# Performance work log

Measured on AMD Instinct MI355X. Metric: run time of the kernel, lower is better.

The kernel has to match this reference:

```python
import jax, jax.numpy as jnp
import numpy as np

N_NODES = 50000
N_EDGES = 800000
IN_CH = 128
OUT_CH = 32
HID = 2 * OUT_CH  # 64


def setup_inputs() -> dict:
    key = jax.random.key(0)
    ks = jax.random.split(key, 8)
    x = jax.random.normal(ks[0], (N_NODES, IN_CH), dtype=jnp.float32)
    edge_index = jax.random.randint(ks[1], (2, N_EDGES), 0, N_NODES, dtype=jnp.int32)
    s1 = 1.0 / np.sqrt(IN_CH)
    s2 = 1.0 / np.sqrt(HID)
    W1 = jax.random.normal(ks[2], (IN_CH, HID), dtype=jnp.float32) * s1
    b1 = jnp.zeros((HID,), dtype=jnp.float32)
    W_mu = jax.random.normal(ks[3], (HID, OUT_CH), dtype=jnp.float32) * s2
    b_mu = jnp.zeros((OUT_CH,), dtype=jnp.float32)
    W_logstd = jax.random.normal(ks[4], (HID, OUT_CH), dtype=jnp.float32) * s2
    b_logstd = jnp.zeros((OUT_CH,), dtype=jnp.float32)
    return {"x": x, "edge_index": edge_index, "W1": W1, "b1": b1,
            "W_mu": W_mu, "b_mu": b_mu, "W_logstd": W_logstd, "b_logstd": b_logstd}


def _gcn_norm(edge_index, n, dtype):
    # PyG GCNConv: add self-loops, symmetric normalization D^-1/2 A D^-1/2
    loops = jnp.arange(n, dtype=edge_index.dtype)
    src = jnp.concatenate([edge_index[0], loops])
    dst = jnp.concatenate([edge_index[1], loops])
    deg = jax.ops.segment_sum(jnp.ones_like(dst, dtype=dtype), dst, num_segments=n)
    deg_inv_sqrt = jnp.where(deg > 0, jax.lax.rsqrt(deg), 0.0)
    norm = deg_inv_sqrt[src] * deg_inv_sqrt[dst]  # [E+N]
    return src, dst, norm


def _gcn_conv(x, W, b, src, dst, norm, n):
    h = x @ W                        # transform first (in >= out)
    msg = h[src] * norm[:, None]     # gather + scale, [E+N, out]
    out = jax.ops.segment_sum(msg, dst, num_segments=n)
    return out + b


def reference(x, edge_index, W1, b1, W_mu, b_mu, W_logstd, b_logstd):
    n = x.shape[0]
    src, dst, norm = _gcn_norm(edge_index, n, x.dtype)
    h = jax.nn.relu(_gcn_conv(x, W1, b1, src, dst, norm, n))
    mu = _gcn_conv(h, W_mu, b_mu, src, dst, norm, n)
    logstd = _gcn_conv(h, W_logstd, b_logstd, src, dst, norm, n)
    return mu, logstd
```

## Files before the change

### kernel.cpp

```cpp
#include <hip/hip_runtime.h>
#include <hip/hip_fp16.h>

#define N_NODES 50000
#define N_EDGES 800000
#define IN_CH 128
#define HID 64
#define OUT_CH 32
#define CAP 64
#define ZROW N_NODES
#define PART_SZ 6250

union H4 { uint2 u; __half2 h[2]; };

__global__ __launch_bounds__(256) void k_scatter(const int* __restrict__ ei,
                                                 int* cur, unsigned short* __restrict__ pk,
                                                 unsigned* zA, unsigned* zB) {
    if (blockIdx.x == 0) {
        int t = threadIdx.x;
        if (t < 32) zA[t] = 0u;
        else if (t < 64) zB[t - 32] = 0u;
    }
    int part = blockIdx.x & 7;
    int g = (blockIdx.x >> 3) * 256 + threadIdx.x;
    if (g >= N_EDGES / 2) return;
    int2 dd = ((const int2*)(ei + N_EDGES))[g];
    bool a0 = (unsigned)(dd.x - part * PART_SZ) < (unsigned)PART_SZ;
    bool a1 = (unsigned)(dd.y - part * PART_SZ) < (unsigned)PART_SZ;
    if (!a0 && !a1) return;
    int2 ss = ((const int2*)ei)[g];
    if (a0) {
        int n = atomicAdd(&cur[dd.x], 1);
        int slot = (n < 32) ? (((n & 7) << 2) | (n >> 3)) : n;
        pk[(dd.x << 6) + slot] = (unsigned short)ss.x;
    }
    if (a1) {
        int n = atomicAdd(&cur[dd.y], 1);
        int slot = (n < 32) ? (((n & 7) << 2) | (n >> 3)) : n;
        pk[(dd.y << 6) + slot] = (unsigned short)ss.y;
    }
}

__global__ __launch_bounds__(256) void k_mm1(const float* __restrict__ x,
                                             const float* __restrict__ W1,
                                             const int* __restrict__ cur,
                                             __half* __restrict__ t1) {
    __shared__ float4 ws[64 * 16];
    __shared__ float  xsT[64 * 64];
    int t = threadIdx.x;
    int n0 = blockIdx.x * 64;
    int lane = t & 63, wv_ = t >> 6;
    int ni = lane >> 2;
    int cq = ((lane & 3) << 2) + wv_;
    const float4* W4 = (const float4*)W1;
    const float4* x4 = (const float4*)x;
    float4 acc0 = {0,0,0,0}, acc1 = acc0, acc2 = acc0, acc3 = acc0;
#pragma unroll
    for (int kt = 0; kt < 2; ++kt) {
        __syncthreads();
#pragma unroll
        for (int i = 0; i < 4; ++i) {
            int L = i * 256 + t;
            ws[L] = W4[kt * 1024 + L];
            int n = L >> 4, q = L & 15;
            int ng = n0 + n; if (ng >= N_NODES) ng = N_NODES - 1;
            float4 v = x4[ng * 32 + kt * 16 + q];
            int fb = q * 256 + (((n >> 2) ^ q) << 2) + (n & 3);
            xsT[fb]       = v.x;
            xsT[fb + 64]  = v.y;
            xsT[fb + 128] = v.z;
            xsT[fb + 192] = v.w;
        }
        __syncthreads();
        const float4* xsT4 = (const float4*)xsT;
#pragma unroll 8
        for (int k = 0; k < 64; ++k) {
            float4 xv = xsT4[k * 16 + (ni ^ (k >> 2))];
            float4 wvv = ws[k * 16 + cq];
            acc0.x += xv.x * wvv.x; acc0.y += xv.x * wvv.y; acc0.z += xv.x * wvv.z; acc0.w += xv.x * wvv.w;
            acc1.x += xv.y * wvv.x; acc1.y += xv.y * wvv.y; acc1.z += xv.y * wvv.z; acc1.w += xv.y * wvv.w;
            acc2.x += xv.z * wvv.x; acc2.y += xv.z * wvv.y; acc2.z += xv.z * wvv.z; acc2.w += xv.z * wvv.w;
            acc3.x += xv.w * wvv.x; acc3.y += xv.w * wvv.y; acc3.z += xv.w * wvv.z; acc3.w += xv.w * wvv.w;
        }
    }
    int nb = n0 + 4 * ni;
    if (nb < N_NODES) {
        int4 c4 = *(const int4*)(cur + nb);
        float d0 = rsqrtf((float)c4.x + 1.0f);
        float d1 = rsqrtf((float)c4.y + 1.0f);
        float d2 = rsqrtf((float)c4.z + 1.0f);
        float d3 = rsqrtf((float)c4.w + 1.0f);
        uint2* o2 = (uint2*)t1;
        H4 v;
        v.h[0] = __floats2half2_rn(d0 * acc0.x, d0 * acc0.y);
        v.h[1] = __floats2half2_rn(d0 * acc0.z, d0 * acc0.w);
        o2[(nb + 0) * 16 + cq] = v.u;
        v.h[0] = __floats2half2_rn(d1 * acc1.x, d1 * acc1.y);
        v.h[1] = __floats2half2_rn(d1 * acc1.z, d1 * acc1.w);
        o2[(nb + 1) * 16 + cq] = v.u;
        v.h[0] = __floats2half2_rn(d2 * acc2.x, d2 * acc2.y);
        v.h[1] = __floats2half2_rn(d2 * acc2.z, d2 * acc2.w);
        o2[(nb + 2) * 16 + cq] = v.u;
        v.h[0] = __floats2half2_rn(d3 * acc3.x, d3 * acc3.y);
        v.h[1] = __floats2half2_rn(d3 * acc3.z, d3 * acc3.w);
        o2[(nb + 3) * 16 + cq] = v.u;
    }
}

__global__ __launch_bounds__(256) void k_agg(const unsigned short* __restrict__ pk,
                                             const int* __restrict__ cur,
                                             const __half* __restrict__ in,
                                             const float* __restrict__ bias,
                                             __half* __restrict__ out,
                                             int apply_relu) {
    int w = (blockIdx.x * 256 + threadIdx.x) >> 6;
    if (w >= N_NODES) return;
    int lane = threadIdx.x & 63;
    int eg = lane >> 3, cs = lane & 7;
    int cnt = __builtin_amdgcn_readfirstlane(cur[w]);
    int rowb = w << 6;
    const uint4* __restrict__ inv = (const uint4*)in;
    float acc[8] = {0,0,0,0,0,0,0,0};

    uint2 pp = *(const uint2*)(pk + rowb + (eg << 2));
    int s0 = (eg      < cnt) ? (int)(pp.x & 0xffff) : ZROW;
    int s1 = (8 + eg  < cnt) ? (int)(pp.x >> 16)    : ZROW;
    int s2 = (16 + eg < cnt) ? (int)(pp.y & 0xffff) : ZROW;
    int s3 = (24 + eg < cnt) ? (int)(pp.y >> 16)    : ZROW;
    uint4 r0 = inv[s0 * 8 + cs];
    uint4 r1 = inv[s1 * 8 + cs];
    uint4 r2 = inv[s2 * 8 + cs];
    uint4 r3 = inv[s3 * 8 + cs];
#define ACC8(R) { const __half2* h2 = (const __half2*)&(R); float2 f;          \
        f = __half22float2(h2[0]); acc[0] += f.x; acc[1] += f.y;               \
        f = __half22float2(h2[1]); acc[2] += f.x; acc[3] += f.y;               \
        f = __half22float2(h2[2]); acc[4] += f.x; acc[5] += f.y;               \
        f = __half22float2(h2[3]); acc[6] += f.x; acc[7] += f.y; }
    ACC8(r0); ACC8(r1); ACC8(r2); ACC8(r3);

    for (int base = 32; base < cnt; base += 8) {
        int je = base + eg;
        int s = (je < cnt) ? (int)pk[rowb + je] : ZROW;
        uint4 r = inv[s * 8 + cs];
        ACC8(r);
    }
#undef ACC8
#pragma unroll
    for (int m = 8; m <= 32; m <<= 1)
#pragma unroll
        for (int i = 0; i < 8; ++i) acc[i] += __shfl_xor(acc[i], m, 64);
    if (eg == 0) {
        uint4 sr = inv[w * 8 + cs];
        const __half2* sh = (const __half2*)&sr;
        float2 f;
        f = __half22float2(sh[0]); acc[0] += f.x; acc[1] += f.y;
        f = __half22float2(sh[1]); acc[2] += f.x; acc[3] += f.y;
        f = __half22float2(sh[2]); acc[4] += f.x; acc[5] += f.y;
        f = __half22float2(sh[3]); acc[6] += f.x; acc[7] += f.y;
        float dw = rsqrtf((float)cnt + 1.0f);
        if (apply_relu) {
            float4 b0 = ((const float4*)bias)[2 * cs];
            float4 b1v = ((const float4*)bias)[2 * cs + 1];
            acc[0] = dw * fmaxf(dw * acc[0] + b0.x, 0.f);
            acc[1] = dw * fmaxf(dw * acc[1] + b0.y, 0.f);
            acc[2] = dw * fmaxf(dw * acc[2] + b0.z, 0.f);
            acc[3] = dw * fmaxf(dw * acc[3] + b0.w, 0.f);
            acc[4] = dw * fmaxf(dw * acc[4] + b1v.x, 0.f);
            acc[5] = dw * fmaxf(dw * acc[5] + b1v.y, 0.f);
            acc[6] = dw * fmaxf(dw * acc[6] + b1v.z, 0.f);
            acc[7] = dw * fmaxf(dw * acc[7] + b1v.w, 0.f);
        } else {
#pragma unroll
            for (int i = 0; i < 8; ++i) acc[i] *= dw;
        }
        __half2 o[4];
        o[0] = __floats2half2_rn(acc[0], acc[1]);
        o[1] = __floats2half2_rn(acc[2], acc[3]);
        o[2] = __floats2half2_rn(acc[4], acc[5]);
        o[3] = __floats2half2_rn(acc[6], acc[7]);
        ((uint4*)out)[w * 8 + cs] = *(const uint4*)o;
    }
}

__global__ __launch_bounds__(256) void k_mm2(const __half* __restrict__ agg2,
                                             const float* __restrict__ Wmu,
                                             const float* __restrict__ bmu,
                                             const float* __restrict__ Wls,
                                             const float* __restrict__ bls,
                                             float* __restrict__ out) {
    __shared__ float4 ws[64 * 16];
    __shared__ float  xsT[64 * 64];
    int t = threadIdx.x;
    int n0 = blockIdx.x * 64;
    int lane = t & 63, wv_ = t >> 6;
    int ni = lane >> 2;
    int cq = ((lane & 3) << 2) + wv_;
    const float4* Wm4 = (const float4*)Wmu;
    const float4* Wl4 = (const float4*)Wls;
    const uint2*  x2  = (const uint2*)agg2;
#pragma unroll
    for (int i = 0; i < 4; ++i) {
        int L = i * 256 + t;
        int k = L >> 4, c = L & 15;
        ws[L] = (c < 8) ? Wm4[k * 8 + c] : Wl4[k * 8 + (c - 8)];
        int n = L >> 4, q = L & 15;
        int ng = n0 + n; if (ng >= N_NODES) ng = N_NODES - 1;
        H4 hv; hv.u = x2[ng * 16 + q];
        float2 f0 = __half22float2(hv.h[0]), f1 = __half22float2(hv.h[1]);
        int fb = q * 256 + (((n >> 2) ^ q) << 2) + (n & 3);
        xsT[fb]       = f0.x;
        xsT[fb + 64]  = f0.y;
        xsT[fb + 128] = f1.x;
        xsT[fb + 192] = f1.y;
    }
    float4 b = (cq < 8) ? ((const float4*)bmu)[cq] : ((const float4*)bls)[cq - 8];
    float4 acc0 = b, acc1 = b, acc2 = b, acc3 = b;
    __syncthreads();
    const float4* xsT4 = (const float4*)xsT;
#pragma unroll 8
    for (int k = 0; k < 64; ++k) {
        float4 xv = xsT4[k * 16 + (ni ^ (k >> 2))];
        float4 wvv = ws[k * 16 + cq];
        acc0.x += xv.x * wvv.x; acc0.y += xv.x * wvv.y; acc0.z += xv.x * wvv.z; acc0.w += xv.x * wvv.w;
        acc1.x += xv.y * wvv.x; acc1.y += xv.y * wvv.y; acc1.z += xv.y * wvv.z; acc1.w += xv.y * wvv.w;
        acc2.x += xv.z * wvv.x; acc2.y += xv.z * wvv.y; acc2.z += xv.z * wvv.z; acc2.w += xv.z * wvv.w;
        acc3.x += xv.w * wvv.x; acc3.y += xv.w * wvv.y; acc3.z += xv.w * wvv.z; acc3.w += xv.w * wvv.w;
    }
    int nb = n0 + 4 * ni;
    if (nb < N_NODES) {
        float4* o4 = (float4*)out;
        long base_off = (cq < 8) ? 0 : (long)N_NODES * 8;
        int cq8 = cq & 7;
        o4[base_off + (long)(nb + 0) * 8 + cq8] = acc0;
        o4[base_off + (long)(nb + 1) * 8 + cq8] = acc1;
        o4[base_off + (long)(nb + 2) * 8 + cq8] = acc2;
        o4[base_off + (long)(nb + 3) * 8 + cq8] = acc3;
    }
}

extern "C" void kernel_launch(void* const* d_in, const int* in_sizes, int n_in,
                              void* d_out, int out_size, void* d_ws, size_t ws_size,
                              hipStream_t stream) {
    const float* x   = (const float*)d_in[0];
    const int*   ei  = (const int*)  d_in[1];
    const float* W1  = (const float*)d_in[2];
    const float* b1  = (const float*)d_in[3];
    const float* Wmu = (const float*)d_in[4];
    const float* bmu = (const float*)d_in[5];
    const float* Wls = (const float*)d_in[6];
    const float* bls = (const float*)d_in[7];
    float* out = (float*)d_out;

    int*   cur  = (int*)d_ws;
    unsigned short* pk = (unsigned short*)((int*)d_ws + 50176);
    __half* bufA = (__half*)((int*)d_ws + 1650176);
    __half* bufB = (__half*)((int*)d_ws + 3250304);
    __half* bufC = (__half*)((int*)d_ws + 4850432);

    hipMemsetAsync(d_ws, 0, 200000, stream);
    k_scatter <<<1563 * 8, 256, 0, stream>>>(ei, cur, pk,
                   (unsigned*)(bufA + (size_t)ZROW * HID),
                   (unsigned*)(bufB + (size_t)ZROW * HID));
    k_mm1 <<<782, 256, 0, stream>>>(x, W1, cur, bufA);
    k_agg <<<12500, 256, 0, stream>>>(pk, cur, bufA, b1, bufB, 1);
    k_agg <<<12500, 256, 0, stream>>>(pk, cur, bufB, nullptr, bufC, 0);
    k_mm2 <<<782, 256, 0, stream>>>(bufC, Wmu, bmu, Wls, bls, out);
}
```

Measured before the change: 187.7 us.

## Shrink per-node adjacency slots to 32 and spill extra edges to overflow list

Halves the fixed per-node neighbor slot capacity from 64 to 32 and routes any edges beyond 32 into a global overflow list of packed (dst,src) pairs, which aggregation scans linearly for high-degree nodes. This shrinks the adjacency buffer and its footprint. The self-loop load is also issued earlier, alongside the neighbor gathers. With average in-degree 16, overflow is rare, but any node with more than 32 in-edges forces a full scan of the overflow list, and only one lane group does that work.

Result: no change. 190.3 us (+1.4%).

```diff
diff --git a/kernel.cpp b/kernel.cpp
--- a/kernel.cpp
+++ b/kernel.cpp
@@ -6,7 +6,7 @@
 #define IN_CH 128
 #define HID 64
 #define OUT_CH 32
-#define CAP 64
+#define CAP 32
 #define ZROW N_NODES
 #define PART_SZ 6250
 
@@ -14,6 +14,7 @@
 
 __global__ __launch_bounds__(256) void k_scatter(const int* __restrict__ ei,
                                                  int* cur, unsigned short* __restrict__ pk,
+                                                 unsigned* ovf,
                                                  unsigned* zA, unsigned* zB) {
     if (blockIdx.x == 0) {
         int t = threadIdx.x;
@@ -30,13 +31,13 @@
     int2 ss = ((const int2*)ei)[g];
     if (a0) {
         int n = atomicAdd(&cur[dd.x], 1);
-        int slot = (n < 32) ? (((n & 7) << 2) | (n >> 3)) : n;
-        pk[(dd.x << 6) + slot] = (unsigned short)ss.x;
+        if (n < 32) pk[(dd.x << 5) + (((n & 7) << 2) | (n >> 3))] = (unsigned short)ss.x;
+        else { int o = atomicAdd((int*)ovf, 1); ovf[1 + o] = ((unsigned)dd.x << 16) | (unsigned)ss.x; }
     }
     if (a1) {
         int n = atomicAdd(&cur[dd.y], 1);
-        int slot = (n < 32) ? (((n & 7) << 2) | (n >> 3)) : n;
-        pk[(dd.y << 6) + slot] = (unsigned short)ss.y;
+        if (n < 32) pk[(dd.y << 5) + (((n & 7) << 2) | (n >> 3))] = (unsigned short)ss.y;
+        else { int o = atomicAdd((int*)ovf, 1); ovf[1 + o] = ((unsigned)dd.y << 16) | (unsigned)ss.y; }
     }
 }
 
@@ -108,6 +109,7 @@
 
 __global__ __launch_bounds__(256) void k_agg(const unsigned short* __restrict__ pk,
                                              const int* __restrict__ cur,
+                                             const unsigned* __restrict__ ovf,
                                              const __half* __restrict__ in,
                                              const float* __restrict__ bias,
                                              __half* __restrict__ out,
@@ -117,11 +119,10 @@
     int lane = threadIdx.x & 63;
     int eg = lane >> 3, cs = lane & 7;
     int cnt = __builtin_amdgcn_readfirstlane(cur[w]);
-    int rowb = w << 6;
     const uint4* __restrict__ inv = (const uint4*)in;
     float acc[8] = {0,0,0,0,0,0,0,0};
 
-    uint2 pp = *(const uint2*)(pk + rowb + (eg << 2));
+    uint2 pp = *(const uint2*)(pk + (w << 5) + (eg << 2));
     int s0 = (eg      < cnt) ? (int)(pp.x & 0xffff) : ZROW;
     int s1 = (8 + eg  < cnt) ? (int)(pp.x >> 16)    : ZROW;
     int s2 = (16 + eg < cnt) ? (int)(pp.y & 0xffff) : ZROW;
@@ -130,18 +131,24 @@
     uint4 r1 = inv[s1 * 8 + cs];
     uint4 r2 = inv[s2 * 8 + cs];
     uint4 r3 = inv[s3 * 8 + cs];
+    uint4 rs = inv[w * 8 + cs];
 #define ACC8(R) { const __half2* h2 = (const __half2*)&(R); float2 f;          \
         f = __half22float2(h2[0]); acc[0] += f.x; acc[1] += f.y;               \
         f = __half22float2(h2[1]); acc[2] += f.x; acc[3] += f.y;               \
         f = __half22float2(h2[2]); acc[4] += f.x; acc[5] += f.y;               \
         f = __half22float2(h2[3]); acc[6] += f.x; acc[7] += f.y; }
     ACC8(r0); ACC8(r1); ACC8(r2); ACC8(r3);
-
-    for (int base = 32; base < cnt; base += 8) {
-        int je = base + eg;
-        int s = (je < cnt) ? (int)pk[rowb + je] : ZROW;
-        uint4 r = inv[s * 8 + cs];
-        ACC8(r);
+    if (eg == 0) ACC8(rs);
+
+    if (cnt > 32) {
+        int on = __builtin_amdgcn_readfirstlane((int)ovf[0]);
+        for (int o = 0; o < on; ++o) {
+            unsigned e = ovf[1 + o];
+            if ((int)(e >> 16) == w && eg == 0) {
+                uint4 r = inv[(int)(e & 0xffffu) * 8 + cs];
+                ACC8(r);
+            }
+        }
     }
 #undef ACC8
 #pragma unroll
@@ -149,13 +156,6 @@
 #pragma unroll
         for (int i = 0; i < 8; ++i) acc[i] += __shfl_xor(acc[i], m, 64);
     if (eg == 0) {
-        uint4 sr = inv[w * 8 + cs];
-        const __half2* sh = (const __half2*)&sr;
-        float2 f;
-        f = __half22float2(sh[0]); acc[0] += f.x; acc[1] += f.y;
-        f = __half22float2(sh[1]); acc[2] += f.x; acc[3] += f.y;
-        f = __half22float2(sh[2]); acc[4] += f.x; acc[5] += f.y;
-        f = __half22float2(sh[3]); acc[6] += f.x; acc[7] += f.y;
         float dw = rsqrtf((float)cnt + 1.0f);
         if (apply_relu) {
             float4 b0 = ((const float4*)bias)[2 * cs];
@@ -250,18 +250,19 @@
     const float* bls = (const float*)d_in[7];
     float* out = (float*)d_out;
 
-    int*   cur  = (int*)d_ws;
+    int*      cur = (int*)d_ws;
+    unsigned* ovf = (unsigned*)d_ws + 50000;
     unsigned short* pk = (unsigned short*)((int*)d_ws + 50176);
-    __half* bufA = (__half*)((int*)d_ws + 1650176);
-    __half* bufB = (__half*)((int*)d_ws + 3250304);
-    __half* bufC = (__half*)((int*)d_ws + 4850432);
-
-    hipMemsetAsync(d_ws, 0, 200000, stream);
-    k_scatter <<<1563 * 8, 256, 0, stream>>>(ei, cur, pk,
+    __half* bufA = (__half*)((int*)d_ws + 850176);
+    __half* bufB = (__half*)((int*)d_ws + 2450208);
+    __half* bufC = (__half*)((int*)d_ws + 4050240);
+
+    hipMemsetAsync(d_ws, 0, 200704, stream);
+    k_scatter <<<1563 * 8, 256, 0, stream>>>(ei, cur, pk, ovf,
                    (unsigned*)(bufA + (size_t)ZROW * HID),
                    (unsigned*)(bufB + (size_t)ZROW * HID));
     k_mm1 <<<782, 256, 0, stream>>>(x, W1, cur, bufA);
-    k_agg <<<12500, 256, 0, stream>>>(pk, cur, bufA, b1, bufB, 1);
-    k_agg <<<12500, 256, 0, stream>>>(pk, cur, bufB, nullptr, bufC, 0);
+    k_agg <<<12500, 256, 0, stream>>>(pk, cur, ovf, bufA, b1, bufB, 1);
+    k_agg <<<12500, 256, 0, stream>>>(pk, cur, ovf, bufB, nullptr, bufC, 0);
     k_mm2 <<<782, 256, 0, stream>>>(bufC, Wmu, bmu, Wls, bls, out);
 }
```

## Process two nodes per wavefront in aggregation with wider neighbor index loads

Applied to the files above, without the earlier changes.

Each 64-lane wave in the aggregation kernel now handles two destination nodes, with 32 lanes per node split into 4 edge groups instead of 8. The packed neighbor slot layout in the scatter kernel is changed so that each edge group reads 8 contiguous indices with a single 16-byte load. The self-loop row is fetched together with the first eight gathers, and the cross-lane reduction takes one fewer step. The aim is to cut lanes wasted on low-degree nodes and issue more loads up front, at the cost of more registers and a wave-uniform edge count becoming per-half divergent.

Result: no change. 184.4 us, median of 2 (-1.8%).

```diff
diff --git a/kernel.cpp b/kernel.cpp
--- a/kernel.cpp
+++ b/kernel.cpp
@@ -30,12 +30,12 @@
     int2 ss = ((const int2*)ei)[g];
     if (a0) {
         int n = atomicAdd(&cur[dd.x], 1);
-        int slot = (n < 32) ? (((n & 7) << 2) | (n >> 3)) : n;
+        int slot = (n < 32) ? (((n & 3) << 3) | (n >> 2)) : n;
         pk[(dd.x << 6) + slot] = (unsigned short)ss.x;
     }
     if (a1) {
         int n = atomicAdd(&cur[dd.y], 1);
-        int slot = (n < 32) ? (((n & 7) << 2) | (n >> 3)) : n;
+        int slot = (n < 32) ? (((n & 3) << 3) | (n >> 2)) : n;
         pk[(dd.y << 6) + slot] = (unsigned short)ss.y;
     }
 }
@@ -112,50 +112,54 @@
                                              const float* __restrict__ bias,
                                              __half* __restrict__ out,
                                              int apply_relu) {
-    int w = (blockIdx.x * 256 + threadIdx.x) >> 6;
-    if (w >= N_NODES) return;
+    int wave = (blockIdx.x * 256 + threadIdx.x) >> 6;
+    if (wave >= N_NODES / 2) return;
     int lane = threadIdx.x & 63;
-    int eg = lane >> 3, cs = lane & 7;
-    int cnt = __builtin_amdgcn_readfirstlane(cur[w]);
+    int half = lane >> 5;
+    int eg = (lane >> 3) & 3;
+    int cs = lane & 7;
+    int w = wave * 2 + half;
+    int cnt = cur[w];
     int rowb = w << 6;
     const uint4* __restrict__ inv = (const uint4*)in;
+
+    uint4 pp = *(const uint4*)(pk + rowb + (eg << 3));
+    const unsigned short* us = (const unsigned short*)&pp;
+    int sidx[8];
+#pragma unroll
+    for (int j = 0; j < 8; ++j)
+        sidx[j] = (eg + 4 * j < cnt) ? (int)us[j] : ZROW;
+    int sself = (eg == 0) ? w : ZROW;
+    uint4 r0 = inv[sidx[0] * 8 + cs];
+    uint4 r1 = inv[sidx[1] * 8 + cs];
+    uint4 r2 = inv[sidx[2] * 8 + cs];
+    uint4 r3 = inv[sidx[3] * 8 + cs];
+    uint4 r4 = inv[sidx[4] * 8 + cs];
+    uint4 r5 = inv[sidx[5] * 8 + cs];
+    uint4 r6 = inv[sidx[6] * 8 + cs];
+    uint4 r7 = inv[sidx[7] * 8 + cs];
+    uint4 rs = inv[sself * 8 + cs];
     float acc[8] = {0,0,0,0,0,0,0,0};
-
-    uint2 pp = *(const uint2*)(pk + rowb + (eg << 2));
-    int s0 = (eg      < cnt) ? (int)(pp.x & 0xffff) : ZROW;
-    int s1 = (8 + eg  < cnt) ? (int)(pp.x >> 16)    : ZROW;
-    int s2 = (16 + eg < cnt) ? (int)(pp.y & 0xffff) : ZROW;
-    int s3 = (24 + eg < cnt) ? (int)(pp.y >> 16)    : ZROW;
-    uint4 r0 = inv[s0 * 8 + cs];
-    uint4 r1 = inv[s1 * 8 + cs];
-    uint4 r2 = inv[s2 * 8 + cs];
-    uint4 r3 = inv[s3 * 8 + cs];
 #define ACC8(R) { const __half2* h2 = (const __half2*)&(R); float2 f;          \
         f = __half22float2(h2[0]); acc[0] += f.x; acc[1] += f.y;               \
         f = __half22float2(h2[1]); acc[2] += f.x; acc[3] += f.y;               \
         f = __half22float2(h2[2]); acc[4] += f.x; acc[5] += f.y;               \
         f = __half22float2(h2[3]); acc[6] += f.x; acc[7] += f.y; }
     ACC8(r0); ACC8(r1); ACC8(r2); ACC8(r3);
-
-    for (int base = 32; base < cnt; base += 8) {
-        int je = base + eg;
-        int s = (je < cnt) ? (int)pk[rowb + je] : ZROW;
+    ACC8(r4); ACC8(r5); ACC8(r6); ACC8(r7);
+    ACC8(rs);
+
+    for (int n = 32 + eg; n < cnt; n += 4) {
+        int s = (int)pk[rowb + n];
         uint4 r = inv[s * 8 + cs];
         ACC8(r);
     }
 #undef ACC8
 #pragma unroll
-    for (int m = 8; m <= 32; m <<= 1)
+    for (int m = 8; m <= 16; m <<= 1)
 #pragma unroll
         for (int i = 0; i < 8; ++i) acc[i] += __shfl_xor(acc[i], m, 64);
     if (eg == 0) {
-        uint4 sr = inv[w * 8 + cs];
-        const __half2* sh = (const __half2*)&sr;
-        float2 f;
-        f = __half22float2(sh[0]); acc[0] += f.x; acc[1] += f.y;
-        f = __half22float2(sh[1]); acc[2] += f.x; acc[3] += f.y;
-        f = __half22float2(sh[2]); acc[4] += f.x; acc[5] += f.y;
-        f = __half22float2(sh[3]); acc[6] += f.x; acc[7] += f.y;
         float dw = rsqrtf((float)cnt + 1.0f);
         if (apply_relu) {
             float4 b0 = ((const float4*)bias)[2 * cs];
@@ -261,7 +265,7 @@
                    (unsigned*)(bufA + (size_t)ZROW * HID),
                    (unsigned*)(bufB + (size_t)ZROW * HID));
     k_mm1 <<<782, 256, 0, stream>>>(x, W1, cur, bufA);
-    k_agg <<<12500, 256, 0, stream>>>(pk, cur, bufA, b1, bufB, 1);
-    k_agg <<<12500, 256, 0, stream>>>(pk, cur, bufB, nullptr, bufC, 0);
+    k_agg <<<6250, 256, 0, stream>>>(pk, cur, bufA, b1, bufB, 1);
+    k_agg <<<6250, 256, 0, stream>>>(pk, cur, bufB, nullptr, bufC, 0);
     k_mm2 <<<782, 256, 0, stream>>>(bufC, Wmu, bmu, Wls, bls, out);
 }
```
